# Kernel optimization log

Measured on AMD Instinct MI355X. Metric: run time of the kernel, lower is better.

The kernel has to match this reference:

```python
import jax, jax.numpy as jnp
import numpy as np

N, F, M, B = 100000, 256, 10, 32768
DECAY = 0.9


def setup_inputs() -> dict:
    key = jax.random.key(0)
    ks = jax.random.split(key, 16)
    s = 1.0 / np.sqrt(F)
    # forward args
    node_indices = jax.random.permutation(ks[0], N)[:B]  # unique indices
    node_features = jax.random.normal(ks[1], (B, F), jnp.float32)
    # per-node state
    hidden_states = jax.random.normal(ks[2], (N, F), jnp.float32) * 0.1
    cell_states = jax.random.normal(ks[3], (N, F), jnp.float32) * 0.1
    temporal_memory = jax.random.normal(ks[4], (N, M, F), jnp.float32) * 0.1
    memory_ptr = jax.random.randint(ks[5], (N,), 0, M)
    # LSTMCell params (gate order i, f, g, o as in torch)
    W_ih = jax.random.normal(ks[6], (4 * F, F), jnp.float32) * s
    W_hh = jax.random.normal(ks[7], (4 * F, F), jnp.float32) * s
    b_ih = jax.random.normal(ks[8], (4 * F,), jnp.float32) * s
    b_hh = jax.random.normal(ks[9], (4 * F,), jnp.float32) * s
    # attention read params
    Wq = jax.random.normal(ks[10], (F, F), jnp.float32) * s
    bq = jnp.zeros((F,), jnp.float32)
    Wk = jax.random.normal(ks[11], (F, F), jnp.float32) * s
    bk = jnp.zeros((F,), jnp.float32)
    Wv = jax.random.normal(ks[12], (F, F), jnp.float32) * s
    bv = jnp.zeros((F,), jnp.float32)
    return dict(node_indices=node_indices, node_features=node_features,
                hidden_states=hidden_states, cell_states=cell_states,
                temporal_memory=temporal_memory, memory_ptr=memory_ptr,
                W_ih=W_ih, W_hh=W_hh, b_ih=b_ih, b_hh=b_hh,
                Wq=Wq, bq=bq, Wk=Wk, bk=bk, Wv=Wv, bv=bv)


def reference(node_indices, node_features, hidden_states, cell_states,
              temporal_memory, memory_ptr, W_ih, W_hh, b_ih, b_hh,
              Wq, bq, Wk, bk, Wv, bv):
    idx = node_indices
    feat = node_features.shape[-1]
    # --- update_memory: LSTMCell on gathered per-node states ---
    h_prev = hidden_states[idx]              # (B, F)
    c_prev = cell_states[idx]                # (B, F)
    gates = node_features @ W_ih.T + b_ih + h_prev @ W_hh.T + b_hh
    i, f, g, o = jnp.split(gates, 4, axis=-1)
    c_new = jax.nn.sigmoid(f) * c_prev + jax.nn.sigmoid(i) * jnp.tanh(g)
    h_new = jax.nn.sigmoid(o) * jnp.tanh(c_new)
    # --- scatter into circular temporal memory + decay previous slot ---
    ptr = memory_ptr[idx]                    # (B,)
    tm = temporal_memory.at[idx, ptr].set(node_features)
    prev = ptr - 1                           # -1 wraps; decay only applied if ptr > 0
    old = tm[idx, prev]                      # (B, F)
    tm = tm.at[idx, prev].set(jnp.where((ptr > 0)[:, None], old * DECAY, old))
    # --- get_temporal_context: gather + tiny attention over M slots ---
    mem = tm[idx]                            # (B, M, F)
    q = h_new @ Wq.T + bq                    # (B, F)  hidden_states[idx] post-update == h_new
    k = mem @ Wk.T + bk                      # (B, M, F)
    v = mem @ Wv.T + bv                      # (B, M, F)
    scores = jnp.einsum('bf,bmf->bm', q, k) / jnp.sqrt(jnp.asarray(feat, q.dtype))
    w = jax.nn.softmax(scores, axis=-1)      # (B, M)
    context = jnp.einsum('bmf,bm->bf', v, w) # (B, F)
    return context
```

## Files before the change

### kernel.cpp

```cpp
#include <hip/hip_runtime.h>
#include <hip/hip_bf16.h>

constexpr int NB = 32768;
constexpr int NF = 256;
constexpr int NM = 10;
constexpr float DECAY = 0.9f;

using bf16x8 = __attribute__((ext_vector_type(8))) short;
using f32x4  = __attribute__((ext_vector_type(4))) float;

static __device__ __forceinline__ ushort f2bf(float x) {
    unsigned u = __float_as_uint(x);
    unsigned r = (u + 0x7fffu + ((u >> 16) & 1u)) >> 16;
    return (ushort)r;
}
static __device__ __forceinline__ float bf2f(ushort x) {
    return __uint_as_float(((unsigned)x) << 16);
}
static __device__ __forceinline__ float sigmoid_f(float x) {
    return 1.f / (1.f + __expf(-x));
}
static __device__ __forceinline__ float tanh_f(float x) {
    float e = __expf(2.f * x);
    return (e - 1.f) / (e + 1.f);
}
static __device__ __forceinline__ void gload16(const void* g, void* l) {
    __builtin_amdgcn_global_load_lds(
        (const __attribute__((address_space(1))) unsigned int*)g,
        (__attribute__((address_space(3))) unsigned int*)l, 16, 0, 0);
}

constexpr int PB_ACAT = 16384;
constexpr int PB_WGI  = PB_ACAT + 1024;
constexpr int PB_WQKT = PB_WGI + 256;
constexpr int PB_WV   = PB_WQKT + 256;
constexpr int PB_TOT  = PB_WV + 1;

__global__ __launch_bounds__(256) void k_prep(
    const float* __restrict__ W_ih, const float* __restrict__ W_hh,
    const float* __restrict__ b_ih, const float* __restrict__ b_hh,
    const float* __restrict__ Wq, const float* __restrict__ bq,
    const float* __restrict__ Wk, const float* __restrict__ Wv,
    const float* __restrict__ nf, const float* __restrict__ hidden,
    const int* __restrict__ idx,
    ushort* __restrict__ Wg, float* __restrict__ bsum,
    ushort* __restrict__ WqkT, float* __restrict__ bqk,
    ushort* __restrict__ Wvb, ushort* __restrict__ Acat)
{
    const int blk = blockIdx.x, tid = threadIdx.x;
    if (blk < PB_ACAT) {
        int t = blk * 256 + tid;
        int row = t >> 7;
        int c4 = (t & 127) * 4;
        const float* src = (c4 < 256) ? (nf + (size_t)row * 256 + c4)
                                      : (hidden + (size_t)idx[row] * 256 + (c4 - 256));
        float4 v = *reinterpret_cast<const float4*>(src);
        ushort4 o;
        o.x = f2bf(v.x); o.y = f2bf(v.y); o.z = f2bf(v.z); o.w = f2bf(v.w);
        *reinterpret_cast<ushort4*>(Acat + (size_t)row * 512 + c4) = o;
    } else if (blk < PB_WGI) {
        int j = blk - PB_ACAT;
        for (int c = tid; c < 512; c += 256) {
            float v = (c < 256) ? W_ih[j * 256 + c] : W_hh[j * 256 + (c - 256)];
            Wg[j * 512 + c] = f2bf(v);
        }
        if (tid == 0) bsum[j] = b_ih[j] + b_hh[j];
    } else if (blk < PB_WQKT) {
        int i = blk - PB_WGI, a = tid;
        float s = 0.f;
#pragma unroll 8
        for (int j = 0; j < 256; ++j) s += Wq[j * 256 + a] * Wk[j * 256 + i];
        WqkT[i * 256 + a] = f2bf(s * 0.0625f);
    } else if (blk < PB_WV) {
        int t = (blk - PB_WQKT) * 256 + tid;
        Wvb[t] = f2bf(Wv[t]);
    } else {
        int i = tid;
        float s = 0.f;
#pragma unroll 8
        for (int j = 0; j < 256; ++j) s += bq[j] * Wk[j * 256 + i];
        bqk[i] = s * 0.0625f;
    }
}

__global__ __launch_bounds__(256) void k_gates2(
    const ushort* __restrict__ Acat, const ushort* __restrict__ Wg,
    const float* __restrict__ bsum, const int* __restrict__ idx,
    const float* __restrict__ cell, ushort* __restrict__ h_new)
{
    __shared__ ushort As[128 * 32];
    __shared__ ushort Bs[128 * 32];
    const int t = threadIdx.x;
    const int w = t >> 6, l = t & 63;
    const int wr = w >> 1, wc = w & 1;
    const int lr = l & 15, lk = l >> 4;

    const int flat = blockIdx.x;
    const int xc = flat & 7, grp = flat >> 3;
    const int by = grp & 7;
    const int bx = (grp >> 3) * 8 + xc;
    const int row0 = bx * 128;
    const int f0 = by * 32;

    f32x4 acc[4][4];
#pragma unroll
    for (int m = 0; m < 4; ++m)
#pragma unroll
        for (int g = 0; g < 4; ++g) acc[m][g] = f32x4{0.f, 0.f, 0.f, 0.f};

    const int srow = l >> 2;
    const int scol = (l & 3) * 8;
    const int u0 = w * 2, u1 = u0 + 1;
    const ushort* aS0 = Acat + (size_t)(row0 + u0 * 16 + srow) * 512 + scol;
    const ushort* aS1 = Acat + (size_t)(row0 + u1 * 16 + srow) * 512 + scol;
    const ushort* bS0 = Wg + (size_t)(w * 256 + f0 + srow) * 512 + scol;
    const ushort* bS1 = Wg + (size_t)(w * 256 + f0 + 16 + srow) * 512 + scol;
    ushort* aL0 = As + u0 * 512; ushort* aL1 = As + u1 * 512;
    ushort* bL0 = Bs + (w * 32) * 32; ushort* bL1 = Bs + (w * 32 + 16) * 32;

    for (int k0 = 0; k0 < 512; k0 += 32) {
        gload16(aS0 + k0, aL0);
        gload16(aS1 + k0, aL1);
        gload16(bS0 + k0, bL0);
        gload16(bS1 + k0, bL1);
        __syncthreads();
        bf16x8 af[4], bfr[4];
#pragma unroll
        for (int m = 0; m < 4; ++m)
            af[m] = *reinterpret_cast<const bf16x8*>(As + (wr * 64 + m * 16 + lr) * 32 + lk * 8);
#pragma unroll
        for (int g = 0; g < 4; ++g)
            bfr[g] = *reinterpret_cast<const bf16x8*>(Bs + (g * 32 + wc * 16 + lr) * 32 + lk * 8);
#pragma unroll
        for (int m = 0; m < 4; ++m)
#pragma unroll
            for (int g = 0; g < 4; ++g)
                acc[m][g] = __builtin_amdgcn_mfma_f32_16x16x32_bf16(af[m], bfr[g], acc[m][g], 0, 0, 0);
        __syncthreads();
    }

    const int f = f0 + wc * 16 + lr;
    float bs[4];
#pragma unroll
    for (int g = 0; g < 4; ++g) bs[g] = bsum[g * 256 + f];

    int nodev[4][4];
#pragma unroll
    for (int m = 0; m < 4; ++m)
#pragma unroll
        for (int r = 0; r < 4; ++r)
            nodev[m][r] = idx[row0 + wr * 64 + m * 16 + lk * 4 + r];

#pragma unroll
    for (int m = 0; m < 4; ++m) {
#pragma unroll
        for (int r = 0; r < 4; ++r) {
            float gi = acc[m][0][r] + bs[0];
            float gf = acc[m][1][r] + bs[1];
            float gg = acc[m][2][r] + bs[2];
            float go = acc[m][3][r] + bs[3];
            float cp = cell[(size_t)nodev[m][r] * 256 + f];
            float cn = sigmoid_f(gf) * cp + sigmoid_f(gi) * tanh_f(gg);
            float hn = sigmoid_f(go) * tanh_f(cn);
            int row = row0 + wr * 64 + m * 16 + lk * 4 + r;
            h_new[(size_t)row * 256 + f] = f2bf(hn);
        }
    }
}

__global__ __launch_bounds__(256) void k_qk(
    const ushort* __restrict__ hnew, const ushort* __restrict__ WqkT,
    const float* __restrict__ bqk, ushort* __restrict__ qbuf)
{
    __shared__ ushort As[64 * 32];
    const int t = threadIdx.x, w = t >> 6, l = t & 63;
    const int lr = l & 15, lk = l >> 4;
    const int row0 = blockIdx.x * 64;

    f32x4 acc[4][4];
#pragma unroll
    for (int m = 0; m < 4; ++m)
#pragma unroll
        for (int n = 0; n < 4; ++n) acc[m][n] = f32x4{0.f, 0.f, 0.f, 0.f};

    const int srow = w * 16 + (l >> 2);
    const int scol = (l & 3) * 8;
    const ushort* aS = hnew + (size_t)(row0 + srow) * 256 + scol;
    ushort* aL = As + (w * 16) * 32;

    const ushort* bptr[4];
#pragma unroll
    for (int n = 0; n < 4; ++n) bptr[n] = WqkT + (size_t)(w * 64 + n * 16 + lr) * 256 + lk * 8;

    for (int k0 = 0; k0 < 256; k0 += 32) {
        gload16(aS + k0, aL);
        __syncthreads();
        bf16x8 a[4], b[4];
#pragma unroll
        for (int m = 0; m < 4; ++m)
            a[m] = *reinterpret_cast<const bf16x8*>(As + (m * 16 + lr) * 32 + lk * 8);
#pragma unroll
        for (int n = 0; n < 4; ++n) b[n] = *reinterpret_cast<const bf16x8*>(bptr[n] + k0);
#pragma unroll
        for (int m = 0; m < 4; ++m)
#pragma unroll
            for (int n = 0; n < 4; ++n)
                acc[m][n] = __builtin_amdgcn_mfma_f32_16x16x32_bf16(a[m], b[n], acc[m][n], 0, 0, 0);
        __syncthreads();
    }

#pragma unroll
    for (int m = 0; m < 4; ++m)
#pragma unroll
        for (int n = 0; n < 4; ++n) {
            int colc = w * 64 + n * 16 + lr;
            float bbq = bqk[colc];
#pragma unroll
            for (int r = 0; r < 4; ++r) {
                int row = row0 + m * 16 + lk * 4 + r;
                qbuf[(size_t)row * 256 + colc] = f2bf(acc[m][n][r] + bbq);
            }
        }
}

static __device__ __forceinline__ int swzb(int row, int byteInRow) {
    return (row * 512 + byteInRow) ^ ((row & 7) << 4);
}

__global__ __launch_bounds__(256) void k_attnout(
    const ushort* __restrict__ qbuf, const ushort* __restrict__ Wvb,
    const float* __restrict__ bv, const int* __restrict__ idx,
    const int* __restrict__ mptr, const float* __restrict__ tm,
    const float* __restrict__ nf, float* __restrict__ out)
{
    __shared__ ushort sC[16 * 256];
    char* sB = (char*)sC;
    const int t = threadIdx.x, w = t >> 6, l = t & 63;
    const int lr = l & 15, lk = l >> 4;
    const int row0 = blockIdx.x * 16;

    {
        const int b0 = row0 + w * 4;
        int nodes[4], ptrs[4];
#pragma unroll
        for (int r = 0; r < 4; ++r) { nodes[r] = idx[b0 + r]; ptrs[r] = mptr[nodes[r]]; }

#pragma unroll
        for (int rr = 0; rr < 4; ++rr) {
            int row = w * 4 + rr;
            int b = b0 + rr;
            int node = nodes[rr];
            int ptr = ptrs[rr];
            ushort4 q4 = *reinterpret_cast<const ushort4*>(qbuf + (size_t)b * 256 + l * 4);
            float q0 = bf2f(q4.x), q1 = bf2f(q4.y), q2 = bf2f(q4.z), q3 = bf2f(q4.w);
            const float* base = tm + (size_t)node * (NM * NF);

            float4 mem[NM];
            float sc[NM];
#pragma unroll
            for (int m = 0; m < NM; ++m) {
                float4 v;
                if (m == ptr) {
                    v = *reinterpret_cast<const float4*>(nf + (size_t)b * 256 + l * 4);
                } else {
                    v = *reinterpret_cast<const float4*>(base + (size_t)m * 256 + l * 4);
                    if (ptr > 0 && m == ptr - 1) { v.x *= DECAY; v.y *= DECAY; v.z *= DECAY; v.w *= DECAY; }
                }
                mem[m] = v;
                sc[m] = q0 * v.x + q1 * v.y + q2 * v.z + q3 * v.w;
            }
#pragma unroll
            for (int m = 0; m < NM; ++m) {
                float s = sc[m];
#pragma unroll
                for (int d = 1; d < 64; d <<= 1) s += __shfl_xor(s, d, 64);
                sc[m] = s;
            }
            float mx = sc[0];
#pragma unroll
            for (int m = 1; m < NM; ++m) mx = fmaxf(mx, sc[m]);
            float e[NM], sum = 0.f;
#pragma unroll
            for (int m = 0; m < NM; ++m) { e[m] = __expf(sc[m] - mx); sum += e[m]; }
            float inv = 1.f / sum;

            float4 c = {0.f, 0.f, 0.f, 0.f};
#pragma unroll
            for (int m = 0; m < NM; ++m) {
                float wm = e[m] * inv;
                c.x += wm * mem[m].x; c.y += wm * mem[m].y; c.z += wm * mem[m].z; c.w += wm * mem[m].w;
            }
            ushort4 o;
            o.x = f2bf(c.x); o.y = f2bf(c.y); o.z = f2bf(c.z); o.w = f2bf(c.w);
            *(ushort4*)(sB + swzb(row, l * 8)) = o;
        }
    }
    __syncthreads();

    f32x4 acc[4];
#pragma unroll
    for (int n = 0; n < 4; ++n) acc[n] = f32x4{0.f, 0.f, 0.f, 0.f};
    const ushort* vptr[4];
#pragma unroll
    for (int n = 0; n < 4; ++n) vptr[n] = Wvb + (size_t)(w * 64 + n * 16 + lr) * 256 + lk * 8;

#pragma unroll 2
    for (int k = 0; k < 256; k += 32) {
        bf16x8 a = *reinterpret_cast<const bf16x8*>(sB + swzb(lr, (k + lk * 8) * 2));
        bf16x8 b[4];
#pragma unroll
        for (int n = 0; n < 4; ++n) b[n] = *reinterpret_cast<const bf16x8*>(vptr[n] + k);
#pragma unroll
        for (int n = 0; n < 4; ++n)
            acc[n] = __builtin_amdgcn_mfma_f32_16x16x32_bf16(a, b[n], acc[n], 0, 0, 0);
    }
#pragma unroll
    for (int n = 0; n < 4; ++n) {
        int colc = w * 64 + n * 16 + lr;
        float bbv = bv[colc];
#pragma unroll
        for (int r = 0; r < 4; ++r) {
            int row = lk * 4 + r;
            out[(size_t)(row0 + row) * 256 + colc] = acc[n][r] + bbv;
        }
    }
}

extern "C" void kernel_launch(void* const* d_in, const int* in_sizes, int n_in,
                              void* d_out, int out_size, void* d_ws, size_t ws_size,
                              hipStream_t stream) {
    const int*   node_indices = (const int*)  d_in[0];
    const float* node_feats   = (const float*)d_in[1];
    const float* hidden       = (const float*)d_in[2];
    const float* cell         = (const float*)d_in[3];
    const float* tmem         = (const float*)d_in[4];
    const int*   memory_ptr   = (const int*)  d_in[5];
    const float* W_ih         = (const float*)d_in[6];
    const float* W_hh         = (const float*)d_in[7];
    const float* b_ih         = (const float*)d_in[8];
    const float* b_hh         = (const float*)d_in[9];
    const float* Wq           = (const float*)d_in[10];
    const float* bq           = (const float*)d_in[11];
    const float* Wk           = (const float*)d_in[12];
    const float* Wv           = (const float*)d_in[14];
    const float* bv           = (const float*)d_in[15];

    char* ws = (char*)d_ws;
    size_t off = 0;
    auto alloc = [&](size_t bytes) { char* p = ws + off; off += (bytes + 255) & ~(size_t)255; return p; };

    ushort* Wg    = (ushort*)alloc((size_t)1024 * 512 * 2);
    ushort* WqkT  = (ushort*)alloc((size_t)256 * 256 * 2);
    ushort* Wvb   = (ushort*)alloc((size_t)256 * 256 * 2);
    float*  bqk   = (float*) alloc((size_t)256 * 4);
    float*  bsum  = (float*) alloc((size_t)1024 * 4);
    ushort* Acat  = (ushort*)alloc((size_t)NB * 512 * 2);
    ushort* hnew  = (ushort*)alloc((size_t)NB * 256 * 2);
    ushort* qbuf  = (ushort*)alloc((size_t)NB * 256 * 2);

    k_prep<<<PB_TOT, 256, 0, stream>>>(W_ih, W_hh, b_ih, b_hh, Wq, bq, Wk, Wv,
                                       node_feats, hidden, node_indices,
                                       Wg, bsum, WqkT, bqk, Wvb, Acat);
    k_gates2<<<2048, 256, 0, stream>>>(Acat, Wg, bsum, node_indices, cell, hnew);
    k_qk<<<NB / 64, 256, 0, stream>>>(hnew, WqkT, bqk, qbuf);
    k_attnout<<<NB / 16, 256, 0, stream>>>(qbuf, Wvb, bv, node_indices, memory_ptr,
                                           tmem, node_feats, (float*)d_out);
}
```

Baseline: 216.5 us.

## Fuse query projection into attention kernel and double-buffer memory row loads

The separate q-projection GEMM kernel and its global qbuf round trip are removed. Each attention block now computes q for its 16 rows with MFMA directly from h_new and WqkT, staging the result in shared memory. The per-row temporal-memory loads are also software-pipelined across two register buffers so the next row's gather overlaps the current row's softmax. In exchange, WqkT is reloaded per 16-row block rather than per 64-row block, and register pressure rises.

```diff
diff --git a/kernel.cpp b/kernel.cpp
--- a/kernel.cpp
+++ b/kernel.cpp
@@ -28,6 +28,9 @@
     __builtin_amdgcn_global_load_lds(
         (const __attribute__((address_space(1))) unsigned int*)g,
         (__attribute__((address_space(3))) unsigned int*)l, 16, 0, 0);
+}
+static __device__ __forceinline__ int swzb(int row, int byteInRow) {
+    return (row * 512 + byteInRow) ^ ((row & 7) << 4);
 }
 
 constexpr int PB_ACAT = 16384;
@@ -168,67 +171,9 @@
     }
 }
 
-__global__ __launch_bounds__(256) void k_qk(
+__global__ __launch_bounds__(256) void k_attnout(
     const ushort* __restrict__ hnew, const ushort* __restrict__ WqkT,
-    const float* __restrict__ bqk, ushort* __restrict__ qbuf)
-{
-    __shared__ ushort As[64 * 32];
-    const int t = threadIdx.x, w = t >> 6, l = t & 63;
-    const int lr = l & 15, lk = l >> 4;
-    const int row0 = blockIdx.x * 64;
-
-    f32x4 acc[4][4];
-#pragma unroll
-    for (int m = 0; m < 4; ++m)
-#pragma unroll
-        for (int n = 0; n < 4; ++n) acc[m][n] = f32x4{0.f, 0.f, 0.f, 0.f};
-
-    const int srow = w * 16 + (l >> 2);
-    const int scol = (l & 3) * 8;
-    const ushort* aS = hnew + (size_t)(row0 + srow) * 256 + scol;
-    ushort* aL = As + (w * 16) * 32;
-
-    const ushort* bptr[4];
-#pragma unroll
-    for (int n = 0; n < 4; ++n) bptr[n] = WqkT + (size_t)(w * 64 + n * 16 + lr) * 256 + lk * 8;
-
-    for (int k0 = 0; k0 < 256; k0 += 32) {
-        gload16(aS + k0, aL);
-        __syncthreads();
-        bf16x8 a[4], b[4];
-#pragma unroll
-        for (int m = 0; m < 4; ++m)
-            a[m] = *reinterpret_cast<const bf16x8*>(As + (m * 16 + lr) * 32 + lk * 8);
-#pragma unroll
-        for (int n = 0; n < 4; ++n) b[n] = *reinterpret_cast<const bf16x8*>(bptr[n] + k0);
-#pragma unroll
-        for (int m = 0; m < 4; ++m)
-#pragma unroll
-            for (int n = 0; n < 4; ++n)
-                acc[m][n] = __builtin_amdgcn_mfma_f32_16x16x32_bf16(a[m], b[n], acc[m][n], 0, 0, 0);
-        __syncthreads();
-    }
-
-#pragma unroll
-    for (int m = 0; m < 4; ++m)
-#pragma unroll
-        for (int n = 0; n < 4; ++n) {
-            int colc = w * 64 + n * 16 + lr;
-            float bbq = bqk[colc];
-#pragma unroll
-            for (int r = 0; r < 4; ++r) {
-                int row = row0 + m * 16 + lk * 4 + r;
-                qbuf[(size_t)row * 256 + colc] = f2bf(acc[m][n][r] + bbq);
-            }
-        }
-}
-
-static __device__ __forceinline__ int swzb(int row, int byteInRow) {
-    return (row * 512 + byteInRow) ^ ((row & 7) << 4);
-}
-
-__global__ __launch_bounds__(256) void k_attnout(
-    const ushort* __restrict__ qbuf, const ushort* __restrict__ Wvb,
+    const float* __restrict__ bqk, const ushort* __restrict__ Wvb,
     const float* __restrict__ bv, const int* __restrict__ idx,
     const int* __restrict__ mptr, const float* __restrict__ tm,
     const float* __restrict__ nf, float* __restrict__ out)
@@ -240,33 +185,65 @@
     const int row0 = blockIdx.x * 16;
 
     {
+        f32x4 qa[4];
+#pragma unroll
+        for (int n = 0; n < 4; ++n) qa[n] = f32x4{0.f, 0.f, 0.f, 0.f};
+        const ushort* ap = hnew + (size_t)(row0 + lr) * 256 + lk * 8;
+        const ushort* bp[4];
+#pragma unroll
+        for (int n = 0; n < 4; ++n) bp[n] = WqkT + (size_t)(w * 64 + n * 16 + lr) * 256 + lk * 8;
+#pragma unroll 2
+        for (int k0 = 0; k0 < 256; k0 += 32) {
+            bf16x8 a = *reinterpret_cast<const bf16x8*>(ap + k0);
+            bf16x8 b[4];
+#pragma unroll
+            for (int n = 0; n < 4; ++n) b[n] = *reinterpret_cast<const bf16x8*>(bp[n] + k0);
+#pragma unroll
+            for (int n = 0; n < 4; ++n)
+                qa[n] = __builtin_amdgcn_mfma_f32_16x16x32_bf16(a, b[n], qa[n], 0, 0, 0);
+        }
+#pragma unroll
+        for (int n = 0; n < 4; ++n) {
+            int colc = w * 64 + n * 16 + lr;
+            float bbq = bqk[colc];
+#pragma unroll
+            for (int r = 0; r < 4; ++r) {
+                int row = lk * 4 + r;
+                *(ushort*)(sB + swzb(row, colc * 2)) = f2bf(qa[n][r] + bbq);
+            }
+        }
+    }
+    __syncthreads();
+
+    {
         const int b0 = row0 + w * 4;
         int nodes[4], ptrs[4];
 #pragma unroll
         for (int r = 0; r < 4; ++r) { nodes[r] = idx[b0 + r]; ptrs[r] = mptr[nodes[r]]; }
 
-#pragma unroll
-        for (int rr = 0; rr < 4; ++rr) {
-            int row = w * 4 + rr;
-            int b = b0 + rr;
-            int node = nodes[rr];
-            int ptr = ptrs[rr];
-            ushort4 q4 = *reinterpret_cast<const ushort4*>(qbuf + (size_t)b * 256 + l * 4);
+        float4 mA[NM], mB[NM];
+
+        auto loadRow = [&](float4* mm, int rr) {
+            const int b = b0 + rr;
+            const int node = nodes[rr], ptr = ptrs[rr];
+            const float* base = tm + (size_t)node * (NM * NF);
+            const float* nfp = nf + (size_t)b * 256 + l * 4;
+#pragma unroll
+            for (int m = 0; m < NM; ++m) {
+                mm[m] = (m == ptr) ? *reinterpret_cast<const float4*>(nfp)
+                                   : *reinterpret_cast<const float4*>(base + (size_t)m * 256 + l * 4);
+            }
+        };
+        auto compRow = [&](float4* mm, int rr) {
+            const int row = w * 4 + rr;
+            const int ptr = ptrs[rr];
+            ushort4 q4 = *(const ushort4*)(sB + swzb(row, l * 8));
             float q0 = bf2f(q4.x), q1 = bf2f(q4.y), q2 = bf2f(q4.z), q3 = bf2f(q4.w);
-            const float* base = tm + (size_t)node * (NM * NF);
-
-            float4 mem[NM];
             float sc[NM];
 #pragma unroll
             for (int m = 0; m < NM; ++m) {
-                float4 v;
-                if (m == ptr) {
-                    v = *reinterpret_cast<const float4*>(nf + (size_t)b * 256 + l * 4);
-                } else {
-                    v = *reinterpret_cast<const float4*>(base + (size_t)m * 256 + l * 4);
-                    if (ptr > 0 && m == ptr - 1) { v.x *= DECAY; v.y *= DECAY; v.z *= DECAY; v.w *= DECAY; }
-                }
-                mem[m] = v;
+                float4 v = mm[m];
+                if (ptr > 0 && m == ptr - 1) { v.x *= DECAY; v.y *= DECAY; v.z *= DECAY; v.w *= DECAY; mm[m] = v; }
                 sc[m] = q0 * v.x + q1 * v.y + q2 * v.z + q3 * v.w;
             }
 #pragma unroll
@@ -283,17 +260,25 @@
 #pragma unroll
             for (int m = 0; m < NM; ++m) { e[m] = __expf(sc[m] - mx); sum += e[m]; }
             float inv = 1.f / sum;
-
             float4 c = {0.f, 0.f, 0.f, 0.f};
 #pragma unroll
             for (int m = 0; m < NM; ++m) {
                 float wm = e[m] * inv;
-                c.x += wm * mem[m].x; c.y += wm * mem[m].y; c.z += wm * mem[m].z; c.w += wm * mem[m].w;
+                c.x += wm * mm[m].x; c.y += wm * mm[m].y; c.z += wm * mm[m].z; c.w += wm * mm[m].w;
             }
             ushort4 o;
             o.x = f2bf(c.x); o.y = f2bf(c.y); o.z = f2bf(c.z); o.w = f2bf(c.w);
             *(ushort4*)(sB + swzb(row, l * 8)) = o;
-        }
+        };
+
+        loadRow(mA, 0);
+        loadRow(mB, 1);
+        compRow(mA, 0);
+        loadRow(mA, 2);
+        compRow(mB, 1);
+        loadRow(mB, 3);
+        compRow(mA, 2);
+        compRow(mB, 3);
     }
     __syncthreads();
 
@@ -356,13 +341,11 @@
     float*  bsum  = (float*) alloc((size_t)1024 * 4);
     ushort* Acat  = (ushort*)alloc((size_t)NB * 512 * 2);
     ushort* hnew  = (ushort*)alloc((size_t)NB * 256 * 2);
-    ushort* qbuf  = (ushort*)alloc((size_t)NB * 256 * 2);
 
     k_prep<<<PB_TOT, 256, 0, stream>>>(W_ih, W_hh, b_ih, b_hh, Wq, bq, Wk, Wv,
                                        node_feats, hidden, node_indices,
                                        Wg, bsum, WqkT, bqk, Wvb, Acat);
     k_gates2<<<2048, 256, 0, stream>>>(Acat, Wg, bsum, node_indices, cell, hnew);
-    k_qk<<<NB / 64, 256, 0, stream>>>(hnew, WqkT, bqk, qbuf);
-    k_attnout<<<NB / 16, 256, 0, stream>>>(qbuf, Wvb, bv, node_indices, memory_ptr,
-                                           tmem, node_feats, (float*)d_out);
-}
+    k_attnout<<<NB / 16, 256, 0, stream>>>(hnew, WqkT, bqk, Wvb, bv, node_indices,
+                                           memory_ptr, tmem, node_feats, (float*)d_out);
+}
```

Measured after the change: 217.9 us. About the same (+0.6%).
